# Kernel tuning notes

Hardware: AMD Instinct MI355X
Metric: run time of the kernel (lower is better)

The kernel has to match this reference:

```python
import jax, jax.numpy as jnp
import numpy as np

N_NODES = 200000
D_IN = 512
HID = 512
D_OUT = 256
B = 1024
SIZES = (25, 10)


def setup_inputs() -> dict:
    key = jax.random.key(0)
    ks = jax.random.split(key, 8)
    x = jax.random.normal(ks[0], (N_NODES, D_IN), dtype=jnp.float32)
    nodes = jax.random.randint(ks[1], (B,), 0, N_NODES)
    neigh1 = jax.random.randint(ks[2], (B * SIZES[0],), 0, N_NODES)
    neigh2 = jax.random.randint(ks[3], (B * SIZES[0] * SIZES[1],), 0, N_NODES)
    # SAGEAggregator weights, stored as [in, out] (torch Linear weight transposed); bias=False
    s = 0.05
    Ws0 = jax.random.normal(ks[4], (D_IN, HID), dtype=jnp.float32) * s
    Wn0 = jax.random.normal(ks[5], (D_IN, HID), dtype=jnp.float32) * s
    Ws1 = jax.random.normal(ks[6], (2 * HID, D_OUT), dtype=jnp.float32) * s
    Wn1 = jax.random.normal(ks[7], (2 * HID, D_OUT), dtype=jnp.float32) * s
    return {"x": x, "nodes": nodes, "neigh1": neigh1, "neigh2": neigh2,
            "Ws0": Ws0, "Wn0": Wn0, "Ws1": Ws1, "Wn1": Wn1}


def _sage_agg(h_self, h_neigh, Ws, Wn, concat):
    # h_self: [M, d], h_neigh: [M, fanout, d] -> mean aggregate then linear transforms
    m = jnp.mean(h_neigh, axis=1)
    a = h_self @ Ws
    b = m @ Wn
    return jnp.concatenate([a, b], axis=-1) if concat else a + b


def reference(x, nodes, neigh1, neigh2, Ws0, Wn0, Ws1, Wn1):
    # gather features for root nodes and sampled 1-hop / 2-hop neighborhoods
    h0 = x[nodes]    # [B, D_IN]
    h1 = x[neigh1]   # [B*25, D_IN]
    h2 = x[neigh2]   # [B*25*10, D_IN]
    d = D_IN
    # layer 0 (concat=True), act=relu, dropout is identity (inference)
    h0 = jax.nn.relu(_sage_agg(h0, h1.reshape(-1, SIZES[0], d), Ws0, Wn0, True))  # [B, 2*HID]
    h1 = jax.nn.relu(_sage_agg(h1, h2.reshape(-1, SIZES[1], d), Ws0, Wn0, True))  # [B*25, 2*HID]
    d2 = 2 * HID
    # layer 1 (last aggregator, concat=False -> sum), no activation
    out = _sage_agg(h0, h1.reshape(-1, SIZES[0], d2), Ws1, Wn1, False)  # [B, D_OUT]
    return out
```

## Files before the change

### kernel.cpp

```cpp
#include <hip/hip_runtime.h>
#include <hip/hip_bf16.h>


#define DEVINL __device__ __forceinline__

typedef __bf16 bf16x8 __attribute__((ext_vector_type(8)));
typedef float f32x4 __attribute__((ext_vector_type(4)));

DEVINL unsigned short f2bf(float f) {
  union { float f; unsigned u; } v; v.f = f;
  unsigned r = v.u + 0x7FFFu + ((v.u >> 16) & 1u);
  return (unsigned short)(r >> 16);
}
DEVINL float bf2f(unsigned short h) {
  union { unsigned u; float f; } v; v.u = ((unsigned)h) << 16;
  return v.f;
}

DEVINL void gload_lds16(const void* g, void* l) {
  __builtin_amdgcn_global_load_lds(
      (const __attribute__((address_space(1))) void*)g,
      (__attribute__((address_space(3))) void*)l, 16, 0, 0);
}

template <int EPI, int BK>
DEVINL void gemm_core(const unsigned short* __restrict__ A, int lda,
                      const unsigned short* __restrict__ Bt, int ldb,
                      int Kc, long tm, long tn, int col0,
                      unsigned short* __restrict__ C0, float* __restrict__ P,
                      float* __restrict__ out, int ldc,
                      unsigned short* As, unsigned short* Bs) {
  const int t = threadIdx.x;
  const int w = t >> 6;
  const int l = t & 63;
  const int wm = w >> 1, wn = w & 1;
  f32x4 acc[4][4] = {};
  constexpr int LPR = BK / 8;
  constexpr int RPW = 64 / LPR;
  constexpr int ROUNDS = 128 / (4 * RPW);
  constexpr int NS = BK / 32;
  const int s_r = l / LPR;
  const int s_kc = (l % LPR) * 8;

  for (int kt = 0; kt < Kc; kt += BK) {
    __syncthreads();
    #pragma unroll
    for (int r = 0; r < ROUNDS; ++r) {
      const int chunk = r * (4 * RPW) + w * RPW;
      gload_lds16(A + (size_t)(tm + chunk + s_r) * lda + kt + s_kc, As + chunk * BK);
      gload_lds16(Bt + (size_t)(tn + chunk + s_r) * ldb + kt + s_kc, Bs + chunk * BK);
    }
    __syncthreads();

    bf16x8 af[4][NS], bfr[4][NS];
    const unsigned short* Ab = As + ((size_t)(wm * 64 + (l & 15)) * BK + (l >> 4) * 8);
    const unsigned short* Bb = Bs + ((size_t)(wn * 64 + (l & 15)) * BK + (l >> 4) * 8);
    #pragma unroll
    for (int f = 0; f < 4; ++f)
      #pragma unroll
      for (int s = 0; s < NS; ++s) {
        af[f][s] = *reinterpret_cast<const bf16x8*>(Ab + f * 16 * BK + s * 32);
        bfr[f][s] = *reinterpret_cast<const bf16x8*>(Bb + f * 16 * BK + s * 32);
      }
    #pragma unroll
    for (int s = 0; s < NS; ++s)
      #pragma unroll
      for (int i = 0; i < 4; ++i)
        #pragma unroll
        for (int j = 0; j < 4; ++j)
          acc[i][j] = __builtin_amdgcn_mfma_f32_16x16x32_bf16(af[i][s], bfr[j][s], acc[i][j], 0, 0, 0);
  }

  const int q = l >> 4, cl = l & 15;
  if (EPI == 0) {
    if (tm < 25600) {
      const int wmBase = (int)tm + wm * 64;
      const int g0w = wmBase / 25;
      float gacc[4][4] = {};
      #pragma unroll
      for (int i = 0; i < 4; ++i)
        #pragma unroll
        for (int r = 0; r < 4; ++r) {
          const int gl = (wmBase + i * 16 + q * 4 + r) / 25 - g0w;
          #pragma unroll
          for (int j = 0; j < 4; ++j) {
            const float v = fmaxf(acc[i][j][r], 0.f);
            #pragma unroll
            for (int slot = 0; slot < 4; ++slot)
              gacc[j][slot] += (gl == slot) ? v : 0.f;
          }
        }
      #pragma unroll
      for (int j = 0; j < 4; ++j)
        #pragma unroll
        for (int slot = 0; slot < 4; ++slot) {
          float v = gacc[j][slot];
          v += __shfl_xor(v, 16);
          v += __shfl_xor(v, 32);
          gacc[j][slot] = v;
        }
      if (q == 0) {
        const int wh = wmBase >> 6;
        #pragma unroll
        for (int slot = 0; slot < 4; ++slot)
          #pragma unroll
          for (int j = 0; j < 4; ++j)
            P[((size_t)wh * 4 + slot) * 1024 + col0 + tn + wn * 64 + j * 16 + cl] = gacc[j][slot];
      }
    } else {
      #pragma unroll
      for (int i = 0; i < 4; ++i)
        #pragma unroll
        for (int j = 0; j < 4; ++j)
          #pragma unroll
          for (int r = 0; r < 4; ++r) {
            const long row = tm - 25600 + wm * 64 + i * 16 + q * 4 + r;
            const long col = col0 + tn + wn * 64 + j * 16 + cl;
            C0[row * 1024 + col] = f2bf(fmaxf(acc[i][j][r], 0.f));
          }
    }
  } else {
    #pragma unroll
    for (int i = 0; i < 4; ++i)
      #pragma unroll
      for (int j = 0; j < 4; ++j)
        #pragma unroll
        for (int r = 0; r < 4; ++r) {
          const long row = tm + wm * 64 + i * 16 + q * 4 + r;
          const long col = tn + wn * 64 + j * 16 + cl;
          atomicAdd(out + row * ldc + col, acc[i][j][r]);
        }
  }
}

DEVINL void xcd_tile_map(int b, long& tm, long& tn) {
  const int xcd = b & 7, idx = b >> 3;
  tm = (long)(xcd + 8 * (idx >> 2)) * 128;
  tn = (long)(idx & 3) * 128;
}

DEVINL void mean10_row(const float* __restrict__ x, const int* __restrict__ neigh2,
                       unsigned short* __restrict__ Hmall, int row, int tid) {
  int c4 = (tid & 127) << 2;
  float4 acc = {0.f, 0.f, 0.f, 0.f};
  const int* ip = neigh2 + (size_t)row * 10;
  #pragma unroll
  for (int j = 0; j < 10; ++j) {
    const float4 v = *reinterpret_cast<const float4*>(x + (size_t)ip[j] * 512 + c4);
    acc.x += v.x; acc.y += v.y; acc.z += v.z; acc.w += v.w;
  }
  const float s = 0.1f;
  ushort4 o; o.x = f2bf(acc.x * s); o.y = f2bf(acc.y * s);
  o.z = f2bf(acc.z * s); o.w = f2bf(acc.w * s);
  *reinterpret_cast<ushort4*>(Hmall + (size_t)row * 512 + c4) = o;
}

__global__ __launch_bounds__(256) void phase0_kernel(
    const float* __restrict__ x, const int* __restrict__ neigh1, const int* __restrict__ nodes,
    const float* __restrict__ Ws0, const float* __restrict__ Wn0,
    const float* __restrict__ Ws1, const float* __restrict__ Wn1,
    unsigned short* __restrict__ Hall,
    unsigned short* __restrict__ WT0s, unsigned short* __restrict__ WT0n,
    unsigned short* __restrict__ WT1s, unsigned short* __restrict__ WT1n,
    float* __restrict__ out) {
  const int b = blockIdx.x;
  const int tid = threadIdx.x;
  if (b < 13312) {
    int row = b * 2 + (tid >> 7);
    int src = row < 25600 ? neigh1[row] : nodes[row - 25600];
    int c4 = (tid & 127) << 2;
    const float4 v = *reinterpret_cast<const float4*>(x + (size_t)src * 512 + c4);
    ushort4 o; o.x = f2bf(v.x); o.y = f2bf(v.y); o.z = f2bf(v.z); o.w = f2bf(v.w);
    *reinterpret_cast<ushort4*>(Hall + (size_t)row * 512 + c4) = o;
  } else if (b < 13312 + 4096) {
    int t = (b - 13312) * 256 + tid;
    int region = t >> 18, local = t & 262143;
    const float* W; unsigned short* WT;
    if (region == 0)      { W = Ws0; WT = WT0s; }
    else if (region == 1) { W = Wn0; WT = WT0n; }
    else if (region == 2) { W = Ws1; WT = WT1s; }
    else                  { W = Wn1; WT = WT1n; }
    int k, n, N;
    if (region < 2) { k = local & 511;  n = local >> 9;  N = 512; }
    else            { k = local & 1023; n = local >> 10; N = 256; }
    WT[local] = f2bf(W[(size_t)k * N + n]);
  } else {
    int t = (b - 17408) * 256 + tid;
    reinterpret_cast<float4*>(out)[t] = float4{0.f, 0.f, 0.f, 0.f};
  }
}

__global__ __launch_bounds__(256) void phase1_kernel(
    const float* __restrict__ x, const int* __restrict__ neigh2,
    const unsigned short* __restrict__ Hall, const unsigned short* __restrict__ WT0s,
    unsigned short* __restrict__ Hmall,
    unsigned short* __restrict__ C0, float* __restrict__ P) {
  __shared__ __align__(16) unsigned short As[128 * 32];
  __shared__ __align__(16) unsigned short Bs[128 * 32];
  const int b = blockIdx.x;
  const int tid = threadIdx.x;
  if (b < 832) {
    long tm, tn;
    xcd_tile_map(b, tm, tn);
    gemm_core<0, 32>(Hall, 512, WT0s, 512, 512, tm, tn, 0, C0, P, nullptr, 0, As, Bs);
  } else if (b < 832 + 12800) {
    mean10_row(x, neigh2, Hmall, (b - 832) * 2 + (tid >> 7), tid);
  } else {
    int g = (b - 13632) * 2 + (tid >> 7);
    int c4 = (tid & 127) << 2;
    float a0 = 0, a1 = 0, a2 = 0, a3 = 0;
    for (int j = 0; j < 25; ++j) {
      ushort4 v = *reinterpret_cast<const ushort4*>(Hall + ((size_t)g * 25 + j) * 512 + c4);
      a0 += bf2f(v.x); a1 += bf2f(v.y); a2 += bf2f(v.z); a3 += bf2f(v.w);
    }
    const float s = 1.0f / 25.0f;
    ushort4 o; o.x = f2bf(a0 * s); o.y = f2bf(a1 * s); o.z = f2bf(a2 * s); o.w = f2bf(a3 * s);
    *reinterpret_cast<ushort4*>(Hmall + ((size_t)25600 + g) * 512 + c4) = o;
  }
}

__global__ __launch_bounds__(256) void phase2_kernel(
    const unsigned short* __restrict__ Hmall, const unsigned short* __restrict__ WT0n,
    unsigned short* __restrict__ C0, float* __restrict__ P) {
  __shared__ __align__(16) unsigned short As[128 * 32];
  __shared__ __align__(16) unsigned short Bs[128 * 32];
  long tm, tn;
  xcd_tile_map(blockIdx.x, tm, tn);
  gemm_core<0, 32>(Hmall, 512, WT0n, 512, 512, tm, tn, 512, C0, P, nullptr, 0, As, Bs);
}

__global__ __launch_bounds__(256) void phaseD_kernel(
    const float* __restrict__ P, unsigned short* __restrict__ M1,
    const unsigned short* __restrict__ C0, const unsigned short* __restrict__ WT1s,
    float* __restrict__ out) {
  __shared__ __align__(16) unsigned short As[128 * 64];
  __shared__ __align__(16) unsigned short Bs[128 * 64];
  const int b = blockIdx.x;
  if (b < 1024) {
    const int g = b;
    const int c = threadIdx.x << 2;
    const int r0 = g * 25, r1 = g * 25 + 24;
    const int wh0 = r0 >> 6, wh1 = r1 >> 6;
    f32x4 s = {0.f, 0.f, 0.f, 0.f};
    for (int wh = wh0; wh <= wh1; ++wh) {
      const int slot = g - (wh * 64) / 25;
      const f32x4 v = *reinterpret_cast<const f32x4*>(P + ((size_t)wh * 4 + slot) * 1024 + c);
      s[0] += v[0]; s[1] += v[1]; s[2] += v[2]; s[3] += v[3];
    }
    const float sc = 1.0f / 25.0f;
    ushort4 o; o.x = f2bf(s[0] * sc); o.y = f2bf(s[1] * sc);
    o.z = f2bf(s[2] * sc); o.w = f2bf(s[3] * sc);
    *reinterpret_cast<ushort4*>(M1 + (size_t)g * 1024 + c) = o;
  } else {
    const int u = b - 1024;
    const int z = u >> 4, bm = (u >> 1) & 7, bn = u & 1;
    gemm_core<1, 64>(C0 + z * 256, 1024, WT1s + z * 256, 1024, 256,
                     (long)bm * 128, (long)bn * 128, 0, nullptr, nullptr, out, 256, As, Bs);
  }
}

__global__ __launch_bounds__(256) void phaseE_kernel(
    const unsigned short* __restrict__ M1, const unsigned short* __restrict__ WT1n,
    float* __restrict__ out) {
  __shared__ __align__(16) unsigned short As[128 * 64];
  __shared__ __align__(16) unsigned short Bs[128 * 64];
  const int b = blockIdx.x;
  const int z = b >> 4, bm = (b >> 1) & 7, bn = b & 1;
  gemm_core<1, 64>(M1 + z * 256, 1024, WT1n + z * 256, 1024, 256,
                   (long)bm * 128, (long)bn * 128, 0, nullptr, nullptr, out, 256, As, Bs);
}

extern "C" void kernel_launch(void* const* d_in, const int* in_sizes, int n_in,
                              void* d_out, int out_size, void* d_ws, size_t ws_size,
                              hipStream_t stream) {
  const float* x      = (const float*)d_in[0];
  const int*   nodes  = (const int*)d_in[1];
  const int*   neigh1 = (const int*)d_in[2];
  const int*   neigh2 = (const int*)d_in[3];
  const float* Ws0    = (const float*)d_in[4];
  const float* Wn0    = (const float*)d_in[5];
  const float* Ws1    = (const float*)d_in[6];
  const float* Wn1    = (const float*)d_in[7];
  float* out = (float*)d_out;

  char* p = (char*)d_ws;
  unsigned short* WT0s  = (unsigned short*)p; p += (size_t)512 * 512 * 2;
  unsigned short* WT0n  = (unsigned short*)p; p += (size_t)512 * 512 * 2;
  unsigned short* WT1s  = (unsigned short*)p; p += (size_t)256 * 1024 * 2;
  unsigned short* WT1n  = (unsigned short*)p; p += (size_t)256 * 1024 * 2;
  unsigned short* Hall  = (unsigned short*)p; p += (size_t)26624 * 512 * 2;
  unsigned short* Hmall = (unsigned short*)p; p += (size_t)26624 * 512 * 2;
  unsigned short* C0    = (unsigned short*)p; p += (size_t)1024 * 1024 * 2;
  unsigned short* M1    = (unsigned short*)p; p += (size_t)1024 * 1024 * 2;
  float*          P     = (float*)p;          p += (size_t)400 * 4 * 1024 * 4;

  hipLaunchKernelGGL(phase0_kernel, dim3(17664), dim3(256), 0, stream,
                     x, neigh1, nodes, Ws0, Wn0, Ws1, Wn1,
                     Hall, WT0s, WT0n, WT1s, WT1n, out);
  hipLaunchKernelGGL(phase1_kernel, dim3(14144), dim3(256), 0, stream,
                     x, neigh2, Hall, WT0s, Hmall, C0, P);
  hipLaunchKernelGGL(phase2_kernel, dim3(832), dim3(256), 0, stream,
                     Hmall, WT0n, C0, P);
  hipLaunchKernelGGL(phaseD_kernel, dim3(1088), dim3(256), 0, stream,
                     P, M1, C0, WT1s, out);
  hipLaunchKernelGGL(phaseE_kernel, dim3(64), dim3(256), 0, stream,
                     M1, WT1n, out);
}
```

Measured before the change: 170.2 us.

## Fuse partial-sum mean reduction into final GEMM A-tile load, drop phaseE

The final neighbor GEMM now builds its A tile directly from the fp32 partial sums P. It reduces and scales them, converts to bf16, and writes them into LDS, replacing the separate M1 reduction kernel and its bf16 round trip through global memory. The self and neighbor GEMMs of the last layer run as blocks of one launch, which removes a kernel launch. In exchange, each GEMM block redoes the reduction for its tiles, and the A load becomes a synchronous register path instead of an async global-to-LDS load.

```diff
diff --git a/kernel.cpp b/kernel.cpp
--- a/kernel.cpp
+++ b/kernel.cpp
@@ -6,6 +6,7 @@
 
 typedef __bf16 bf16x8 __attribute__((ext_vector_type(8)));
 typedef float f32x4 __attribute__((ext_vector_type(4)));
+typedef unsigned short u16x8 __attribute__((ext_vector_type(8)));
 
 DEVINL unsigned short f2bf(float f) {
   union { float f; unsigned u; } v; v.f = f;
@@ -47,7 +48,28 @@
     #pragma unroll
     for (int r = 0; r < ROUNDS; ++r) {
       const int chunk = r * (4 * RPW) + w * RPW;
-      gload_lds16(A + (size_t)(tm + chunk + s_r) * lda + kt + s_kc, As + chunk * BK);
+      if (EPI != 2) {
+        gload_lds16(A + (size_t)(tm + chunk + s_r) * lda + kt + s_kc, As + chunk * BK);
+      } else {
+        const int g = (int)tm + chunk + s_r;
+        const int k = col0 + kt + s_kc;
+        const int wh0 = (g * 25) >> 6, wh1 = (g * 25 + 24) >> 6;
+        float s0 = 0, s1 = 0, s2 = 0, s3 = 0, s4 = 0, s5 = 0, s6 = 0, s7 = 0;
+        for (int wh = wh0; wh <= wh1; ++wh) {
+          const int slot = g - (wh * 64) / 25;
+          const float* src = P + ((size_t)(wh * 4 + slot)) * 1024 + k;
+          const f32x4 v0 = *reinterpret_cast<const f32x4*>(src);
+          const f32x4 v1 = *reinterpret_cast<const f32x4*>(src + 4);
+          s0 += v0[0]; s1 += v0[1]; s2 += v0[2]; s3 += v0[3];
+          s4 += v1[0]; s5 += v1[1]; s6 += v1[2]; s7 += v1[3];
+        }
+        const float sc = 1.0f / 25.0f;
+        u16x8 hv;
+        hv[0] = f2bf(s0 * sc); hv[1] = f2bf(s1 * sc); hv[2] = f2bf(s2 * sc);
+        hv[3] = f2bf(s3 * sc); hv[4] = f2bf(s4 * sc); hv[5] = f2bf(s5 * sc);
+        hv[6] = f2bf(s6 * sc); hv[7] = f2bf(s7 * sc);
+        *reinterpret_cast<u16x8*>(As + chunk * BK + l * 8) = hv;
+      }
       gload_lds16(Bt + (size_t)(tn + chunk + s_r) * ldb + kt + s_kc, Bs + chunk * BK);
     }
     __syncthreads();
@@ -230,44 +252,22 @@
 }
 
 __global__ __launch_bounds__(256) void phaseD_kernel(
-    const float* __restrict__ P, unsigned short* __restrict__ M1,
     const unsigned short* __restrict__ C0, const unsigned short* __restrict__ WT1s,
+    const unsigned short* __restrict__ WT1n, float* __restrict__ P,
     float* __restrict__ out) {
   __shared__ __align__(16) unsigned short As[128 * 64];
   __shared__ __align__(16) unsigned short Bs[128 * 64];
   const int b = blockIdx.x;
-  if (b < 1024) {
-    const int g = b;
-    const int c = threadIdx.x << 2;
-    const int r0 = g * 25, r1 = g * 25 + 24;
-    const int wh0 = r0 >> 6, wh1 = r1 >> 6;
-    f32x4 s = {0.f, 0.f, 0.f, 0.f};
-    for (int wh = wh0; wh <= wh1; ++wh) {
-      const int slot = g - (wh * 64) / 25;
-      const f32x4 v = *reinterpret_cast<const f32x4*>(P + ((size_t)wh * 4 + slot) * 1024 + c);
-      s[0] += v[0]; s[1] += v[1]; s[2] += v[2]; s[3] += v[3];
-    }
-    const float sc = 1.0f / 25.0f;
-    ushort4 o; o.x = f2bf(s[0] * sc); o.y = f2bf(s[1] * sc);
-    o.z = f2bf(s[2] * sc); o.w = f2bf(s[3] * sc);
-    *reinterpret_cast<ushort4*>(M1 + (size_t)g * 1024 + c) = o;
-  } else {
-    const int u = b - 1024;
-    const int z = u >> 4, bm = (u >> 1) & 7, bn = u & 1;
+  if (b < 64) {
+    const int z = b >> 4, bm = (b >> 1) & 7, bn = b & 1;
     gemm_core<1, 64>(C0 + z * 256, 1024, WT1s + z * 256, 1024, 256,
                      (long)bm * 128, (long)bn * 128, 0, nullptr, nullptr, out, 256, As, Bs);
-  }
-}
-
-__global__ __launch_bounds__(256) void phaseE_kernel(
-    const unsigned short* __restrict__ M1, const unsigned short* __restrict__ WT1n,
-    float* __restrict__ out) {
-  __shared__ __align__(16) unsigned short As[128 * 64];
-  __shared__ __align__(16) unsigned short Bs[128 * 64];
-  const int b = blockIdx.x;
-  const int z = b >> 4, bm = (b >> 1) & 7, bn = b & 1;
-  gemm_core<1, 64>(M1 + z * 256, 1024, WT1n + z * 256, 1024, 256,
-                   (long)bm * 128, (long)bn * 128, 0, nullptr, nullptr, out, 256, As, Bs);
+  } else {
+    const int u = b - 64;
+    const int z = u >> 4, bm = (u >> 1) & 7, bn = u & 1;
+    gemm_core<2, 64>(nullptr, 0, WT1n + z * 256, 1024, 256,
+                     (long)bm * 128, (long)bn * 128, z * 256, nullptr, P, out, 256, As, Bs);
+  }
 }
 
 extern "C" void kernel_launch(void* const* d_in, const int* in_sizes, int n_in,
@@ -291,7 +291,6 @@
   unsigned short* Hall  = (unsigned short*)p; p += (size_t)26624 * 512 * 2;
   unsigned short* Hmall = (unsigned short*)p; p += (size_t)26624 * 512 * 2;
   unsigned short* C0    = (unsigned short*)p; p += (size_t)1024 * 1024 * 2;
-  unsigned short* M1    = (unsigned short*)p; p += (size_t)1024 * 1024 * 2;
   float*          P     = (float*)p;          p += (size_t)400 * 4 * 1024 * 4;
 
   hipLaunchKernelGGL(phase0_kernel, dim3(17664), dim3(256), 0, stream,
@@ -301,8 +300,6 @@
                      x, neigh2, Hall, WT0s, Hmall, C0, P);
   hipLaunchKernelGGL(phase2_kernel, dim3(832), dim3(256), 0, stream,
                      Hmall, WT0n, C0, P);
-  hipLaunchKernelGGL(phaseD_kernel, dim3(1088), dim3(256), 0, stream,
-                     P, M1, C0, WT1s, out);
-  hipLaunchKernelGGL(phaseE_kernel, dim3(64), dim3(256), 0, stream,
-                     M1, WT1n, out);
-}
+  hipLaunchKernelGGL(phaseD_kernel, dim3(128), dim3(256), 0, stream,
+                     C0, WT1s, WT1n, P, out);
+}
```

Result: no change. 173.5 us (+2.0%).
